# Kernel tuning notes

Measured on AMD Instinct MI355X. Metric: run time of the kernel, lower is better.

The kernel has to match this reference:

```python
import jax, jax.numpy as jnp
import numpy as np

NR, NA = 2, 1                 # num_raw, num_angle
QDIM = NR + 2 * NA            # 4: [r, x1=cos(th), x2=sin(th)]
DQ = NR + NA                  # 3: [dr, dth]
D = 2 * NR + 3 * NA           # 7: full state dim
HID = 256
EPS = 1e-6


def setup_inputs() -> dict:
    key = jax.random.key(0)
    ks = jax.random.split(key, 4)
    B = 32768
    x = jax.random.normal(ks[0], (B, D), dtype=jnp.float32)
    W0 = jax.random.normal(ks[1], (HID, D), dtype=jnp.float32) / np.sqrt(D)
    b0 = jnp.zeros((HID,), dtype=jnp.float32)
    W1 = jax.random.normal(ks[2], (HID, HID), dtype=jnp.float32) / np.sqrt(HID)
    b1 = jnp.zeros((HID,), dtype=jnp.float32)
    W2 = jax.random.normal(ks[3], (1, HID), dtype=jnp.float32) / np.sqrt(HID)
    b2 = jnp.zeros((1,), dtype=jnp.float32)
    return {"x": x, "W0": W0, "b0": b0, "W1": W1, "b1": b1, "W2": W2, "b2": b2}


def _lnn_forward(x, W0, b0, W1, b1, W2, b2):
    def L_single(xi):  # scalar Lagrangian of one state (D,)
        h = jnp.tanh(W0 @ xi + b0)
        h = jnp.tanh(W1 @ h + b1)
        return (W2 @ h + b2)[0]

    grad_single = jax.grad(L_single)
    gradL = jax.vmap(grad_single)(x)                       # (B, D)

    # Rows of the Hessian corresponding to d/d(dr,dth): (B, DQ, D).
    # Replaces the torch per-row autograd.grad loop with one batched jacfwd.
    def g(xi):
        return grad_single(xi)[QDIM:]                      # dL/d(dr,dth), (DQ,)
    Hrows = jax.vmap(jax.jacfwd(g))(x)                     # (B, DQ, D)

    x1 = x[:, NR:NR + NA]                                  # cos part (B, NA)
    x2 = x[:, NR + NA:QDIM]                                # sin part (B, NA)

    Jr = Hrows[:, :, :NR]                                  # (B, DQ, NR)
    Jx1 = Hrows[:, :, NR:NR + NA]                          # (B, DQ, NA)
    Jx2 = Hrows[:, :, NR + NA:QDIM]                        # (B, DQ, NA)
    Hdq = Hrows[:, :, QDIM:] + EPS * jnp.eye(DQ, dtype=x.dtype)  # (B, DQ, DQ)

    # chain rule back to angle theta: d/dth = -x2 * d/dx1 + x1 * d/dx2
    Jth = -x2[:, None, :] * Jx1 + x1[:, None, :] * Jx2     # (B, DQ, NA)
    Jrth = jnp.concatenate([Jr, Jth], axis=2)              # (B, DQ, DQ)

    dLdr = gradL[:, :NR]
    dLdx1 = gradL[:, NR:NR + NA]
    dLdx2 = gradL[:, NR + NA:QDIM]
    dLdth = -x2 * dLdx1 + x1 * dLdx2
    dLdrdth = jnp.concatenate([dLdr, dLdth], axis=1)       # (B, DQ)

    dq = x[:, QDIM:]                                       # (B, DQ)
    dq_term = jnp.einsum('bij,bj->bi', Jrth, dq)

    rhs = dLdrdth - dq_term                                # control = 0 (no controlNet)
    ddq = jnp.linalg.solve(Hdq, rhs[..., None])[..., 0]    # (B, DQ)

    dr = dq[:, :NR]
    dth = dq[:, NR:]
    dx1 = -x2 * dth
    dx2 = x1 * dth
    return jnp.concatenate([dr, dx1, dx2, ddq], axis=1)    # (B, D)


def reference(x, W0, b0, W1, b1, W2, b2):
    return _lnn_forward(x, W0, b0, W1, b1, W2, b2)
```

## Files before the change

### kernel.cpp

```cpp
#include <hip/hip_runtime.h>
#include <math.h>

#define HID 256
#define EPS_REG 1e-6

typedef __attribute__((ext_vector_type(8))) short short8;
typedef __attribute__((ext_vector_type(4))) short short4v;
typedef __attribute__((ext_vector_type(4))) float v4f;

#define MFMA_BF16(a, b, c) __builtin_amdgcn_mfma_f32_16x16x32_bf16((a), (b), (c), 0, 0, 0)

__device__ __forceinline__ float rtn_bf16(float v, short* s) {
    unsigned u = __float_as_uint(v);
    unsigned r = (u + 0x7FFFu + ((u >> 16) & 1u)) & 0xFFFF0000u;
    *s = (short)(r >> 16);
    return __uint_as_float(r);
}
__device__ __forceinline__ void split3(float v, short* a, short* b, short* c) {
    float f0 = rtn_bf16(v, a);
    float r1 = v - f0;
    float f1 = rtn_bf16(r1, b);
    float r2 = r1 - f1;
    (void)rtn_bf16(r2, c);
}

__global__ void prep_w1_frags(const float* __restrict__ W1, short* __restrict__ ws) {
    const int gid   = blockIdx.x * 64 + threadIdx.x;
    const int lane  = gid & 63;
    const int ks    = (gid >> 6) & 7;
    const int rt    = (gid >> 9) & 15;
    const int which = gid >> 13;
    const int m = lane & 15, q = lane >> 4;

    float v[8];
    if (which == 0) {
        const float* p = W1 + (size_t)(rt*16 + m)*HID + ks*32 + q*8;
#pragma unroll
        for (int t = 0; t < 8; ++t) v[t] = p[t];
    } else {
        const float* p = W1 + (size_t)(ks*32 + q*8)*HID + rt*16 + m;
#pragma unroll
        for (int t = 0; t < 8; ++t) v[t] = p[(size_t)t*HID];
    }
    short8 h8, m8, l8;
#pragma unroll
    for (int t = 0; t < 8; ++t) {
        short sh, sm, sl;
        split3(v[t], &sh, &sm, &sl);
        h8[t] = sh; m8[t] = sm; l8[t] = sl;
    }
    const size_t base = (size_t)which*3*65536 + ((size_t)(rt*8 + ks)*64 + lane)*8;
    *(short8*)(ws + base)          = h8;
    *(short8*)(ws + base + 65536)  = m8;
    *(short8*)(ws + base + 131072) = l8;
}

#define FRAG_NT_STRIDE 13056
#define FRAG_BUF_STRIDE 4352

__global__ __launch_bounds__(512, 4)
void lnn_mfma(const float* __restrict__ x,
              const float* __restrict__ W0, const float* __restrict__ b0,
              const float* __restrict__ b1, const float* __restrict__ W2,
              const short* __restrict__ ws,
              float* __restrict__ out)
{
    __shared__ __align__(16) short Bfrag[26112];
    __shared__ float M0h[HID * 9];

    const int tid   = threadIdx.x;
    const int samp0 = blockIdx.x * 8;
    const int lane  = tid & 63;
    const int w     = tid >> 6;

    {
        const int j  = tid & 255;
        const int s0 = (tid >> 8) * 4;
        float w0r[7];
#pragma unroll
        for (int d = 0; d < 7; ++d) w0r[d] = W0[j*7 + d];
        const float bj = b0[j];
        const int kbase = (j >> 3)*136 + (j & 7);
#pragma unroll
        for (int si = 0; si < 4; ++si) {
            const int s = s0 + si;
            const float* xs = x + (size_t)(samp0 + s)*7;
            float z = bj;
#pragma unroll
            for (int d = 0; d < 7; ++d) z = fmaf(w0r[d], xs[d], z);
            const float h  = tanhf(z);
            const float sg = 1.0f - h*h;
            M0h[j*9 + s] = h;
            const int nt = s >> 2;
            const int cb = (s & 3) * 4;
            float vals[4] = {h, sg*w0r[4], sg*w0r[5], sg*w0r[6]};
#pragma unroll
            for (int comp = 0; comp < 4; ++comp) {
                short sh, sm, sl;
                split3(vals[comp], &sh, &sm, &sl);
                const int a = nt*FRAG_NT_STRIDE + kbase + (cb + comp)*8;
                Bfrag[a]                    = sh;
                Bfrag[a + FRAG_BUF_STRIDE]  = sm;
                Bfrag[a + 2*FRAG_BUF_STRIDE]= sl;
            }
        }
    }
    __syncthreads();

    const short8* A1h = (const short8*)ws;
    const short8* A1m = A1h + 8192;
    const short8* A1l = A1h + 16384;
    const short8* A2h = A1h + 24576;
    const short8* A2m = A1h + 32768;
    const short8* A2l = A1h + 40960;

    const int q = lane >> 4;
    const int c = lane & 15;
    const int boff = q*136 + c*8;

    v4f acc[2][2];
#pragma unroll
    for (int rtl = 0; rtl < 2; ++rtl)
#pragma unroll
        for (int nt = 0; nt < 2; ++nt) acc[rtl][nt] = (v4f){0.f, 0.f, 0.f, 0.f};

#pragma unroll
    for (int ks = 0; ks < 8; ++ks) {
        short8 bh[2], bm[2], bl[2];
#pragma unroll
        for (int nt = 0; nt < 2; ++nt) {
            const int a = nt*FRAG_NT_STRIDE + ks*544 + boff;
            bh[nt] = *(const short8*)(&Bfrag[a]);
            bm[nt] = *(const short8*)(&Bfrag[a + FRAG_BUF_STRIDE]);
            bl[nt] = *(const short8*)(&Bfrag[a + 2*FRAG_BUF_STRIDE]);
        }
#pragma unroll
        for (int rtl = 0; rtl < 2; ++rtl) {
            const size_t fi = ((size_t)((w*2 + rtl)*8 + ks))*64 + lane;
            const short8 ah = A1h[fi];
            const short8 am = A1m[fi];
            const short8 al = A1l[fi];
#pragma unroll
            for (int nt = 0; nt < 2; ++nt) {
                acc[rtl][nt] = MFMA_BF16(ah, bl[nt], acc[rtl][nt]);
                acc[rtl][nt] = MFMA_BF16(al, bh[nt], acc[rtl][nt]);
                acc[rtl][nt] = MFMA_BF16(am, bm[nt], acc[rtl][nt]);
                acc[rtl][nt] = MFMA_BF16(am, bh[nt], acc[rtl][nt]);
                acc[rtl][nt] = MFMA_BF16(ah, bm[nt], acc[rtl][nt]);
                acc[rtl][nt] = MFMA_BF16(ah, bh[nt], acc[rtl][nt]);
            }
        }
    }
    __syncthreads();

    {
        const int myreg = c & 3;
#pragma unroll
        for (int rtl = 0; rtl < 2; ++rtl) {
            const int base = (w*2 + rtl)*16;
            float b1r[4], w2r[4];
#pragma unroll
            for (int r = 0; r < 4; ++r) {
                b1r[r] = b1[base + q*4 + r];
                w2r[r] = W2[base + q*4 + r];
            }
            const int G  = (base >> 3) + (q >> 1);
            const int tq = (q & 1) * 4;
#pragma unroll
            for (int nt = 0; nt < 2; ++nt) {
                float z0r[4];
#pragma unroll
                for (int r = 0; r < 4; ++r)
                    z0r[r] = __shfl(acc[rtl][nt][r] + b1r[r], lane & ~3, 64);
                const float h1m = tanhf(z0r[myreg]);
                float h1r[4];
#pragma unroll
                for (int r = 0; r < 4; ++r)
                    h1r[r] = __shfl(h1m, (lane & ~3) + r, 64);
                short4v ph, pm, pl;
#pragma unroll
                for (int r = 0; r < 4; ++r) {
                    const float h1 = h1r[r];
                    const float s1 = 1.0f - h1*h1;
                    const float av = acc[rtl][nt][r];
                    const float u  = (myreg == 0) ? (w2r[r]*s1)
                                                  : (-2.0f*w2r[r]*h1*s1)*av;
                    short sh, sm, sl;
                    split3(u, &sh, &sm, &sl);
                    ph[r] = sh; pm[r] = sm; pl[r] = sl;
                }
                const int a = nt*FRAG_NT_STRIDE + G*136 + c*8 + tq;
                *(short4v*)(&Bfrag[a])                     = ph;
                *(short4v*)(&Bfrag[a + FRAG_BUF_STRIDE])   = pm;
                *(short4v*)(&Bfrag[a + 2*FRAG_BUF_STRIDE]) = pl;
            }
        }
    }
    __syncthreads();

    v4f acc2[2][2];
#pragma unroll
    for (int rtl = 0; rtl < 2; ++rtl)
#pragma unroll
        for (int nt = 0; nt < 2; ++nt) acc2[rtl][nt] = (v4f){0.f, 0.f, 0.f, 0.f};

#pragma unroll
    for (int ks = 0; ks < 8; ++ks) {
        short8 bh[2], bm[2], bl[2];
#pragma unroll
        for (int nt = 0; nt < 2; ++nt) {
            const int a = nt*FRAG_NT_STRIDE + ks*544 + boff;
            bh[nt] = *(const short8*)(&Bfrag[a]);
            bm[nt] = *(const short8*)(&Bfrag[a + FRAG_BUF_STRIDE]);
            bl[nt] = *(const short8*)(&Bfrag[a + 2*FRAG_BUF_STRIDE]);
        }
#pragma unroll
        for (int rtl = 0; rtl < 2; ++rtl) {
            const size_t fi = ((size_t)((w*2 + rtl)*8 + ks))*64 + lane;
            const short8 ah = A2h[fi];
            const short8 am = A2m[fi];
            const short8 al = A2l[fi];
#pragma unroll
            for (int nt = 0; nt < 2; ++nt) {
                acc2[rtl][nt] = MFMA_BF16(ah, bl[nt], acc2[rtl][nt]);
                acc2[rtl][nt] = MFMA_BF16(al, bh[nt], acc2[rtl][nt]);
                acc2[rtl][nt] = MFMA_BF16(am, bm[nt], acc2[rtl][nt]);
                acc2[rtl][nt] = MFMA_BF16(am, bh[nt], acc2[rtl][nt]);
                acc2[rtl][nt] = MFMA_BF16(ah, bm[nt], acc2[rtl][nt]);
                acc2[rtl][nt] = MFMA_BF16(ah, bh[nt], acc2[rtl][nt]);
            }
        }
    }
    __syncthreads();

    {
        float* U0 = (float*)Bfrag;
#pragma unroll
        for (int rtl = 0; rtl < 2; ++rtl) {
#pragma unroll
            for (int reg = 0; reg < 4; ++reg) {
                const int j = (w*2 + rtl)*16 + q*4 + reg;
                const float w0sel = W0[j*7 + 3 + (c & 3)];
#pragma unroll
                for (int nt = 0; nt < 2; ++nt) {
                    const int s = nt*4 + (c >> 2);
                    const float pv = acc2[rtl][nt][reg];
                    const float p0 = __shfl(pv, lane & ~3, 64);
                    const float h0 = M0h[j*9 + s];
                    const float sg = 1.0f - h0*h0;
                    const float t2 = -2.0f * p0 * h0 * sg;
                    const float res = ((c & 3) == 0) ? (p0*sg)
                                                     : fmaf(pv, sg, t2 * w0sel);
                    U0[j*36 + s*4 + (c & 3)] = res;
                }
            }
        }
    }
    __syncthreads();

    const float* U0 = (const float*)Bfrag;
    const int s = tid >> 6;
    const int t = tid & 63;
    float part[25];
#pragma unroll
    for (int qq = 0; qq < 25; ++qq) part[qq] = 0.0f;

#pragma unroll
    for (int m = 0; m < 4; ++m) {
        const int j = t + 64*m;
        const float4 uv = *(const float4*)(&U0[j*36 + s*4]);
        float w0d[7];
#pragma unroll
        for (int d = 0; d < 7; ++d) w0d[d] = W0[j*7 + d];
#pragma unroll
        for (int d = 0; d < 4; ++d) part[d] = fmaf(uv.x, w0d[d], part[d]);
#pragma unroll
        for (int d = 0; d < 7; ++d) {
            part[4  + d] = fmaf(uv.y, w0d[d], part[4  + d]);
            part[11 + d] = fmaf(uv.z, w0d[d], part[11 + d]);
            part[18 + d] = fmaf(uv.w, w0d[d], part[18 + d]);
        }
    }
#pragma unroll
    for (int off = 32; off >= 1; off >>= 1)
#pragma unroll
        for (int qq = 0; qq < 25; ++qq)
            part[qq] += __shfl_xor(part[qq], off, 64);

    if (t == 0) {
        const float* xs = x + (size_t)(samp0 + s)*7;
        const double x1 = xs[2], x2 = xs[3];
        const double dq0 = xs[4], dq1 = xs[5], dth = xs[6];

        double A[3][4];
#pragma unroll
        for (int i = 0; i < 3; ++i) {
            const double J0 = part[4 + i*7 + 0];
            const double J1 = part[4 + i*7 + 1];
            const double J2 = -x2*(double)part[4 + i*7 + 2] + x1*(double)part[4 + i*7 + 3];
            const double dL = (i == 0) ? (double)part[0]
                            : (i == 1) ? (double)part[1]
                            : (-x2*(double)part[2] + x1*(double)part[3]);
            A[i][0] = (double)part[4 + i*7 + 4] + (i == 0 ? EPS_REG : 0.0);
            A[i][1] = (double)part[4 + i*7 + 5] + (i == 1 ? EPS_REG : 0.0);
            A[i][2] = (double)part[4 + i*7 + 6] + (i == 2 ? EPS_REG : 0.0);
            A[i][3] = dL - (J0*dq0 + J1*dq1 + J2*dth);
        }
        for (int cc = 0; cc < 2; ++cc) {
            int piv = cc;
            double mx = fabs(A[cc][cc]);
            for (int rr = cc + 1; rr < 3; ++rr) {
                const double v = fabs(A[rr][cc]);
                if (v > mx) { mx = v; piv = rr; }
            }
            if (piv != cc) {
                for (int k2 = 0; k2 < 4; ++k2) {
                    const double tmp = A[cc][k2]; A[cc][k2] = A[piv][k2]; A[piv][k2] = tmp;
                }
            }
            const double inv = 1.0 / A[cc][cc];
            for (int rr = cc + 1; rr < 3; ++rr) {
                const double f = A[rr][cc] * inv;
                for (int k2 = cc + 1; k2 < 4; ++k2) A[rr][k2] -= f * A[cc][k2];
            }
        }
        const double sol2 = A[2][3] / A[2][2];
        const double sol1 = (A[1][3] - A[1][2]*sol2) / A[1][1];
        const double sol0 = (A[0][3] - A[0][1]*sol1 - A[0][2]*sol2) / A[0][0];

        float* o = out + (size_t)(samp0 + s)*7;
        o[0] = (float)dq0;
        o[1] = (float)dq1;
        o[2] = (float)(-x2*dth);
        o[3] = (float)( x1*dth);
        o[4] = (float)sol0;
        o[5] = (float)sol1;
        o[6] = (float)sol2;
    }
}

#define TS8 8
#define SCP 36

__global__ void transpose_w1(const float* __restrict__ W1, float* __restrict__ W1T) {
    __shared__ float tile[32][33];
    const int bx = blockIdx.x & 7;
    const int by = blockIdx.x >> 3;
    const int tx = threadIdx.x & 31;
    const int ty = threadIdx.x >> 5;
#pragma unroll
    for (int q = 0; q < 4; ++q)
        tile[ty + q*8][tx] = W1[(by*32 + ty + q*8)*HID + bx*32 + tx];
    __syncthreads();
#pragma unroll
    for (int q = 0; q < 4; ++q)
        W1T[(bx*32 + ty + q*8)*HID + by*32 + tx] = tile[tx][ty + q*8];
}

__global__ __launch_bounds__(256, 2)
void lnn_fused(const float* __restrict__ x,
               const float* __restrict__ W0, const float* __restrict__ b0,
               const float* __restrict__ W1, const float* __restrict__ b1,
               const float* __restrict__ W2,
               const float* __restrict__ W1T, const int useT,
               float* __restrict__ out)
{
    __shared__ float M0[HID * SCP];
    __shared__ float U [HID * SCP];
    const int tid   = threadIdx.x;
    const int samp0 = blockIdx.x * TS8;
    {
        const int j = tid;
        float w0r[7];
#pragma unroll
        for (int d = 0; d < 7; ++d) w0r[d] = W0[j*7 + d];
        const float bj = b0[j];
#pragma unroll
        for (int s = 0; s < TS8; ++s) {
            const float* xs = x + (size_t)(samp0 + s)*7;
            float z = bj;
#pragma unroll
            for (int d = 0; d < 7; ++d) z = fmaf(w0r[d], xs[d], z);
            const float h  = tanhf(z);
            const float sg = 1.0f - h*h;
            float4 v = {h, sg * w0r[4], sg * w0r[5], sg * w0r[6]};
            *(float4*)(&M0[j*SCP + s*4]) = v;
        }
    }
    __syncthreads();
    const int it = tid & 63;
    const int ct = tid >> 6;
    float acc[4][8];
#pragma unroll
    for (int r = 0; r < 4; ++r)
#pragma unroll
        for (int c = 0; c < 8; ++c) acc[r][c] = 0.0f;
    if (useT) {
#pragma unroll 4
        for (int j = 0; j < HID; ++j) {
            const float4 w4 = *(const float4*)(W1T + (size_t)j*HID + it*4);
            const float4 ma = *(const float4*)(&M0[j*SCP + ct*8]);
            const float4 mb = *(const float4*)(&M0[j*SCP + ct*8 + 4]);
            const float w[4] = {w4.x, w4.y, w4.z, w4.w};
            const float m[8] = {ma.x, ma.y, ma.z, ma.w, mb.x, mb.y, mb.z, mb.w};
#pragma unroll
            for (int r = 0; r < 4; ++r)
#pragma unroll
                for (int c = 0; c < 8; ++c)
                    acc[r][c] = fmaf(w[r], m[c], acc[r][c]);
        }
    } else {
#pragma unroll 2
        for (int j = 0; j < HID; ++j) {
            float w[4];
#pragma unroll
            for (int r = 0; r < 4; ++r) w[r] = W1[(size_t)(it*4 + r)*HID + j];
            const float4 ma = *(const float4*)(&M0[j*SCP + ct*8]);
            const float4 mb = *(const float4*)(&M0[j*SCP + ct*8 + 4]);
            const float m[8] = {ma.x, ma.y, ma.z, ma.w, mb.x, mb.y, mb.z, mb.w};
#pragma unroll
            for (int r = 0; r < 4; ++r)
#pragma unroll
                for (int c = 0; c < 8; ++c)
                    acc[r][c] = fmaf(w[r], m[c], acc[r][c]);
        }
    }
    {
#pragma unroll
        for (int r = 0; r < 4; ++r) {
            const int i = it*4 + r;
            const float b1i = b1[i];
            const float w2i = W2[i];
#pragma unroll
            for (int cs = 0; cs < 2; ++cs) {
                const float z1 = acc[r][cs*4+0] + b1i;
                const float h1 = tanhf(z1);
                const float s1 = 1.0f - h1*h1;
                float4 uv;
                uv.x = w2i * s1;
                const float m2 = -2.0f * w2i * h1 * s1;
                uv.y = m2 * acc[r][cs*4+1];
                uv.z = m2 * acc[r][cs*4+2];
                uv.w = m2 * acc[r][cs*4+3];
                *(float4*)(&U[i*SCP + ct*8 + cs*4]) = uv;
            }
        }
    }
    __syncthreads();
    float acc2[4][8];
#pragma unroll
    for (int r = 0; r < 4; ++r)
#pragma unroll
        for (int c = 0; c < 8; ++c) acc2[r][c] = 0.0f;
#pragma unroll 4
    for (int i = 0; i < HID; ++i) {
        const float4 w4 = *(const float4*)(W1 + (size_t)i*HID + it*4);
        const float4 ua = *(const float4*)(&U[i*SCP + ct*8]);
        const float4 ub = *(const float4*)(&U[i*SCP + ct*8 + 4]);
        const float w[4] = {w4.x, w4.y, w4.z, w4.w};
        const float m[8] = {ua.x, ua.y, ua.z, ua.w, ub.x, ub.y, ub.z, ub.w};
#pragma unroll
        for (int r = 0; r < 4; ++r)
#pragma unroll
            for (int c = 0; c < 8; ++c)
                acc2[r][c] = fmaf(w[r], m[c], acc2[r][c]);
    }
    __syncthreads();
    {
#pragma unroll
        for (int r = 0; r < 4; ++r) {
            const int j = it*4 + r;
#pragma unroll
            for (int cs = 0; cs < 2; ++cs) {
                const int scb = ct*8 + cs*4;
                const float4 mm = *(const float4*)(&M0[j*SCP + scb]);
                const float h0v = mm.x;
                const float sg  = 1.0f - h0v*h0v;
                const float p   = acc2[r][cs*4+0];
                const float t2  = -2.0f * p * h0v;
                float4 uv;
                uv.x = p * sg;
                uv.y = fmaf(acc2[r][cs*4+1], sg, t2 * mm.y);
                uv.z = fmaf(acc2[r][cs*4+2], sg, t2 * mm.z);
                uv.w = fmaf(acc2[r][cs*4+3], sg, t2 * mm.w);
                *(float4*)(&U[j*SCP + scb]) = uv;
            }
        }
    }
    __syncthreads();
    const int s = tid >> 5;
    const int t = tid & 31;
    float part[25];
#pragma unroll
    for (int qq = 0; qq < 25; ++qq) part[qq] = 0.0f;
#pragma unroll
    for (int m = 0; m < 8; ++m) {
        const int j = t + 32*m;
        const float4 uv = *(const float4*)(&U[j*SCP + s*4]);
        float w0d[7];
#pragma unroll
        for (int d = 0; d < 7; ++d) w0d[d] = W0[j*7 + d];
#pragma unroll
        for (int d = 0; d < 4; ++d) part[d] = fmaf(uv.x, w0d[d], part[d]);
#pragma unroll
        for (int d = 0; d < 7; ++d) {
            part[4  + d] = fmaf(uv.y, w0d[d], part[4  + d]);
            part[11 + d] = fmaf(uv.z, w0d[d], part[11 + d]);
            part[18 + d] = fmaf(uv.w, w0d[d], part[18 + d]);
        }
    }
#pragma unroll
    for (int off = 16; off >= 1; off >>= 1)
#pragma unroll
        for (int qq = 0; qq < 25; ++qq)
            part[qq] += __shfl_xor(part[qq], off, 64);
    if (t == 0) {
        const float* xs = x + (size_t)(samp0 + s)*7;
        const double x1 = xs[2], x2 = xs[3];
        const double dq0 = xs[4], dq1 = xs[5], dth = xs[6];
        double A[3][4];
#pragma unroll
        for (int i = 0; i < 3; ++i) {
            const double J0 = part[4 + i*7 + 0];
            const double J1 = part[4 + i*7 + 1];
            const double J2 = -x2*(double)part[4 + i*7 + 2] + x1*(double)part[4 + i*7 + 3];
            const double dL = (i == 0) ? (double)part[0]
                            : (i == 1) ? (double)part[1]
                            : (-x2*(double)part[2] + x1*(double)part[3]);
            A[i][0] = (double)part[4 + i*7 + 4] + (i == 0 ? EPS_REG : 0.0);
            A[i][1] = (double)part[4 + i*7 + 5] + (i == 1 ? EPS_REG : 0.0);
            A[i][2] = (double)part[4 + i*7 + 6] + (i == 2 ? EPS_REG : 0.0);
            A[i][3] = dL - (J0*dq0 + J1*dq1 + J2*dth);
        }
        for (int cc = 0; cc < 2; ++cc) {
            int piv = cc;
            double mx = fabs(A[cc][cc]);
            for (int rr = cc + 1; rr < 3; ++rr) {
                const double v = fabs(A[rr][cc]);
                if (v > mx) { mx = v; piv = rr; }
            }
            if (piv != cc) {
                for (int k2 = 0; k2 < 4; ++k2) {
                    const double tmp = A[cc][k2]; A[cc][k2] = A[piv][k2]; A[piv][k2] = tmp;
                }
            }
            const double inv = 1.0 / A[cc][cc];
            for (int rr = cc + 1; rr < 3; ++rr) {
                const double f = A[rr][cc] * inv;
                for (int k2 = cc + 1; k2 < 4; ++k2) A[rr][k2] -= f * A[cc][k2];
            }
        }
        const double sol2 = A[2][3] / A[2][2];
        const double sol1 = (A[1][3] - A[1][2]*sol2) / A[1][1];
        const double sol0 = (A[0][3] - A[0][1]*sol1 - A[0][2]*sol2) / A[0][0];
        float* o = out + (size_t)(samp0 + s)*7;
        o[0] = (float)dq0;
        o[1] = (float)dq1;
        o[2] = (float)(-x2*dth);
        o[3] = (float)( x1*dth);
        o[4] = (float)sol0;
        o[5] = (float)sol1;
        o[6] = (float)sol2;
    }
}

extern "C" void kernel_launch(void* const* d_in, const int* in_sizes, int n_in,
                              void* d_out, int out_size, void* d_ws, size_t ws_size,
                              hipStream_t stream) {
    const float* x  = (const float*)d_in[0];
    const float* W0 = (const float*)d_in[1];
    const float* b0 = (const float*)d_in[2];
    const float* W1 = (const float*)d_in[3];
    const float* b1 = (const float*)d_in[4];
    const float* W2 = (const float*)d_in[5];
    float* out = (float*)d_out;

    const int B = in_sizes[0] / 7;
    const size_t NEED = 6u * 65536u * sizeof(short);

    if (ws_size >= NEED && (B % 8) == 0) {
        short* ws = (short*)d_ws;
        prep_w1_frags<<<256, 64, 0, stream>>>(W1, ws);
        lnn_mfma<<<B / 8, 512, 0, stream>>>(x, W0, b0, b1, W2, ws, out);
    } else {
        const int useT = (ws_size >= (size_t)HID * HID * sizeof(float)) ? 1 : 0;
        float* W1T = (float*)d_ws;
        if (useT) transpose_w1<<<64, 256, 0, stream>>>(W1, W1T);
        lnn_fused<<<B / TS8, 256, 0, stream>>>(x, W0, b0, W1, b1, W2, W1T, useT, out);
    }
}
```

Measured before the change: 300.1 us.

## Prefetch A fragments, reduce via LDS scratch, use cofactor solve, simplify rounding

The W1/W2 fragment loads from global memory are double-buffered across k-steps so the next step's A fragments load while the current MFMAs run. The 64-lane shuffle reduction of 25 partials is cut to two shuffle steps, with the rest summed through an LDS scratch area. The pivoted Gaussian elimination becomes a closed-form 3x3 cofactor/determinant solve, and bf16 rounding switches from round-to-nearest-even to a cheaper round-half-up. The prefetch raises register pressure, the cofactor solve drops pivoting, and the scratch writes lack an explicit barrier, which relies on intra-wave ordering.

```diff
diff --git a/kernel.cpp b/kernel.cpp
--- a/kernel.cpp
+++ b/kernel.cpp
@@ -11,8 +11,7 @@
 #define MFMA_BF16(a, b, c) __builtin_amdgcn_mfma_f32_16x16x32_bf16((a), (b), (c), 0, 0, 0)
 
 __device__ __forceinline__ float rtn_bf16(float v, short* s) {
-    unsigned u = __float_as_uint(v);
-    unsigned r = (u + 0x7FFFu + ((u >> 16) & 1u)) & 0xFFFF0000u;
+    unsigned r = (__float_as_uint(v) + 0x8000u) & 0xFFFF0000u;
     *s = (short)(r >> 16);
     return __uint_as_float(r);
 }
@@ -124,30 +123,45 @@
 #pragma unroll
         for (int nt = 0; nt < 2; ++nt) acc[rtl][nt] = (v4f){0.f, 0.f, 0.f, 0.f};
 
-#pragma unroll
-    for (int ks = 0; ks < 8; ++ks) {
-        short8 bh[2], bm[2], bl[2];
-#pragma unroll
-        for (int nt = 0; nt < 2; ++nt) {
-            const int a = nt*FRAG_NT_STRIDE + ks*544 + boff;
-            bh[nt] = *(const short8*)(&Bfrag[a]);
-            bm[nt] = *(const short8*)(&Bfrag[a + FRAG_BUF_STRIDE]);
-            bl[nt] = *(const short8*)(&Bfrag[a + 2*FRAG_BUF_STRIDE]);
-        }
+    {
+        short8 pah[2][2], pam[2][2], pal[2][2];
 #pragma unroll
         for (int rtl = 0; rtl < 2; ++rtl) {
-            const size_t fi = ((size_t)((w*2 + rtl)*8 + ks))*64 + lane;
-            const short8 ah = A1h[fi];
-            const short8 am = A1m[fi];
-            const short8 al = A1l[fi];
+            const size_t fi = ((size_t)((w*2 + rtl)*8))*64 + lane;
+            pah[0][rtl] = A1h[fi]; pam[0][rtl] = A1m[fi]; pal[0][rtl] = A1l[fi];
+        }
+#pragma unroll
+        for (int ks = 0; ks < 8; ++ks) {
+            const int cur = ks & 1, nxt = cur ^ 1;
+            if (ks < 7) {
+#pragma unroll
+                for (int rtl = 0; rtl < 2; ++rtl) {
+                    const size_t fi = ((size_t)((w*2 + rtl)*8 + ks + 1))*64 + lane;
+                    pah[nxt][rtl] = A1h[fi]; pam[nxt][rtl] = A1m[fi]; pal[nxt][rtl] = A1l[fi];
+                }
+            }
+            short8 bh[2], bm[2], bl[2];
 #pragma unroll
             for (int nt = 0; nt < 2; ++nt) {
-                acc[rtl][nt] = MFMA_BF16(ah, bl[nt], acc[rtl][nt]);
-                acc[rtl][nt] = MFMA_BF16(al, bh[nt], acc[rtl][nt]);
-                acc[rtl][nt] = MFMA_BF16(am, bm[nt], acc[rtl][nt]);
-                acc[rtl][nt] = MFMA_BF16(am, bh[nt], acc[rtl][nt]);
-                acc[rtl][nt] = MFMA_BF16(ah, bm[nt], acc[rtl][nt]);
-                acc[rtl][nt] = MFMA_BF16(ah, bh[nt], acc[rtl][nt]);
+                const int a = nt*FRAG_NT_STRIDE + ks*544 + boff;
+                bh[nt] = *(const short8*)(&Bfrag[a]);
+                bm[nt] = *(const short8*)(&Bfrag[a + FRAG_BUF_STRIDE]);
+                bl[nt] = *(const short8*)(&Bfrag[a + 2*FRAG_BUF_STRIDE]);
+            }
+#pragma unroll
+            for (int rtl = 0; rtl < 2; ++rtl) {
+                const short8 ah = pah[cur][rtl];
+                const short8 am = pam[cur][rtl];
+                const short8 al = pal[cur][rtl];
+#pragma unroll
+                for (int nt = 0; nt < 2; ++nt) {
+                    acc[rtl][nt] = MFMA_BF16(ah, bl[nt], acc[rtl][nt]);
+                    acc[rtl][nt] = MFMA_BF16(al, bh[nt], acc[rtl][nt]);
+                    acc[rtl][nt] = MFMA_BF16(am, bm[nt], acc[rtl][nt]);
+                    acc[rtl][nt] = MFMA_BF16(am, bh[nt], acc[rtl][nt]);
+                    acc[rtl][nt] = MFMA_BF16(ah, bm[nt], acc[rtl][nt]);
+                    acc[rtl][nt] = MFMA_BF16(ah, bh[nt], acc[rtl][nt]);
+                }
             }
         }
     }
@@ -204,30 +218,45 @@
 #pragma unroll
         for (int nt = 0; nt < 2; ++nt) acc2[rtl][nt] = (v4f){0.f, 0.f, 0.f, 0.f};
 
-#pragma unroll
-    for (int ks = 0; ks < 8; ++ks) {
-        short8 bh[2], bm[2], bl[2];
-#pragma unroll
-        for (int nt = 0; nt < 2; ++nt) {
-            const int a = nt*FRAG_NT_STRIDE + ks*544 + boff;
-            bh[nt] = *(const short8*)(&Bfrag[a]);
-            bm[nt] = *(const short8*)(&Bfrag[a + FRAG_BUF_STRIDE]);
-            bl[nt] = *(const short8*)(&Bfrag[a + 2*FRAG_BUF_STRIDE]);
-        }
+    {
+        short8 pah[2][2], pam[2][2], pal[2][2];
 #pragma unroll
         for (int rtl = 0; rtl < 2; ++rtl) {
-            const size_t fi = ((size_t)((w*2 + rtl)*8 + ks))*64 + lane;
-            const short8 ah = A2h[fi];
-            const short8 am = A2m[fi];
-            const short8 al = A2l[fi];
+            const size_t fi = ((size_t)((w*2 + rtl)*8))*64 + lane;
+            pah[0][rtl] = A2h[fi]; pam[0][rtl] = A2m[fi]; pal[0][rtl] = A2l[fi];
+        }
+#pragma unroll
+        for (int ks = 0; ks < 8; ++ks) {
+            const int cur = ks & 1, nxt = cur ^ 1;
+            if (ks < 7) {
+#pragma unroll
+                for (int rtl = 0; rtl < 2; ++rtl) {
+                    const size_t fi = ((size_t)((w*2 + rtl)*8 + ks + 1))*64 + lane;
+                    pah[nxt][rtl] = A2h[fi]; pam[nxt][rtl] = A2m[fi]; pal[nxt][rtl] = A2l[fi];
+                }
+            }
+            short8 bh[2], bm[2], bl[2];
 #pragma unroll
             for (int nt = 0; nt < 2; ++nt) {
-                acc2[rtl][nt] = MFMA_BF16(ah, bl[nt], acc2[rtl][nt]);
-                acc2[rtl][nt] = MFMA_BF16(al, bh[nt], acc2[rtl][nt]);
-                acc2[rtl][nt] = MFMA_BF16(am, bm[nt], acc2[rtl][nt]);
-                acc2[rtl][nt] = MFMA_BF16(am, bh[nt], acc2[rtl][nt]);
-                acc2[rtl][nt] = MFMA_BF16(ah, bm[nt], acc2[rtl][nt]);
-                acc2[rtl][nt] = MFMA_BF16(ah, bh[nt], acc2[rtl][nt]);
+                const int a = nt*FRAG_NT_STRIDE + ks*544 + boff;
+                bh[nt] = *(const short8*)(&Bfrag[a]);
+                bm[nt] = *(const short8*)(&Bfrag[a + FRAG_BUF_STRIDE]);
+                bl[nt] = *(const short8*)(&Bfrag[a + 2*FRAG_BUF_STRIDE]);
+            }
+#pragma unroll
+            for (int rtl = 0; rtl < 2; ++rtl) {
+                const short8 ah = pah[cur][rtl];
+                const short8 am = pam[cur][rtl];
+                const short8 al = pal[cur][rtl];
+#pragma unroll
+                for (int nt = 0; nt < 2; ++nt) {
+                    acc2[rtl][nt] = MFMA_BF16(ah, bl[nt], acc2[rtl][nt]);
+                    acc2[rtl][nt] = MFMA_BF16(al, bh[nt], acc2[rtl][nt]);
+                    acc2[rtl][nt] = MFMA_BF16(am, bm[nt], acc2[rtl][nt]);
+                    acc2[rtl][nt] = MFMA_BF16(am, bh[nt], acc2[rtl][nt]);
+                    acc2[rtl][nt] = MFMA_BF16(ah, bm[nt], acc2[rtl][nt]);
+                    acc2[rtl][nt] = MFMA_BF16(ah, bh[nt], acc2[rtl][nt]);
+                }
             }
         }
     }
@@ -259,7 +288,8 @@
     __syncthreads();
 
     const float* U0 = (const float*)Bfrag;
-    const int s = tid >> 6;
+    float* scratch = ((float*)Bfrag) + 9216 + w * 425;
+    const int s = w;
     const int t = tid & 63;
     float part[25];
 #pragma unroll
@@ -282,51 +312,62 @@
         }
     }
 #pragma unroll
-    for (int off = 32; off >= 1; off >>= 1)
+    for (int off = 1; off <= 2; off <<= 1)
 #pragma unroll
         for (int qq = 0; qq < 25; ++qq)
             part[qq] += __shfl_xor(part[qq], off, 64);
+    {
+        const int quad = t >> 2;
+        if ((t & 3) == 0) {
+#pragma unroll
+            for (int e = 0; e < 25; ++e)
+                scratch[e*17 + quad] = part[e];
+        }
+    }
+    if (t < 25) {
+        float tot = 0.0f;
+#pragma unroll
+        for (int k = 0; k < 16; ++k) tot += scratch[t*17 + k];
+        scratch[t*17 + 16] = tot;
+    }
 
     if (t == 0) {
+        double g[25];
+#pragma unroll
+        for (int e = 0; e < 25; ++e) g[e] = (double)scratch[e*17 + 16];
+
         const float* xs = x + (size_t)(samp0 + s)*7;
         const double x1 = xs[2], x2 = xs[3];
         const double dq0 = xs[4], dq1 = xs[5], dth = xs[6];
 
-        double A[3][4];
+        double M[3][3], rhs[3];
 #pragma unroll
         for (int i = 0; i < 3; ++i) {
-            const double J0 = part[4 + i*7 + 0];
-            const double J1 = part[4 + i*7 + 1];
-            const double J2 = -x2*(double)part[4 + i*7 + 2] + x1*(double)part[4 + i*7 + 3];
-            const double dL = (i == 0) ? (double)part[0]
-                            : (i == 1) ? (double)part[1]
-                            : (-x2*(double)part[2] + x1*(double)part[3]);
-            A[i][0] = (double)part[4 + i*7 + 4] + (i == 0 ? EPS_REG : 0.0);
-            A[i][1] = (double)part[4 + i*7 + 5] + (i == 1 ? EPS_REG : 0.0);
-            A[i][2] = (double)part[4 + i*7 + 6] + (i == 2 ? EPS_REG : 0.0);
-            A[i][3] = dL - (J0*dq0 + J1*dq1 + J2*dth);
-        }
-        for (int cc = 0; cc < 2; ++cc) {
-            int piv = cc;
-            double mx = fabs(A[cc][cc]);
-            for (int rr = cc + 1; rr < 3; ++rr) {
-                const double v = fabs(A[rr][cc]);
-                if (v > mx) { mx = v; piv = rr; }
-            }
-            if (piv != cc) {
-                for (int k2 = 0; k2 < 4; ++k2) {
-                    const double tmp = A[cc][k2]; A[cc][k2] = A[piv][k2]; A[piv][k2] = tmp;
-                }
-            }
-            const double inv = 1.0 / A[cc][cc];
-            for (int rr = cc + 1; rr < 3; ++rr) {
-                const double f = A[rr][cc] * inv;
-                for (int k2 = cc + 1; k2 < 4; ++k2) A[rr][k2] -= f * A[cc][k2];
-            }
-        }
-        const double sol2 = A[2][3] / A[2][2];
-        const double sol1 = (A[1][3] - A[1][2]*sol2) / A[1][1];
-        const double sol0 = (A[0][3] - A[0][1]*sol1 - A[0][2]*sol2) / A[0][0];
+            const double J0 = g[4 + i*7 + 0];
+            const double J1 = g[4 + i*7 + 1];
+            const double J2 = -x2*g[4 + i*7 + 2] + x1*g[4 + i*7 + 3];
+            const double dL = (i == 0) ? g[0]
+                            : (i == 1) ? g[1]
+                            : (-x2*g[2] + x1*g[3]);
+            M[i][0] = g[4 + i*7 + 4] + (i == 0 ? EPS_REG : 0.0);
+            M[i][1] = g[4 + i*7 + 5] + (i == 1 ? EPS_REG : 0.0);
+            M[i][2] = g[4 + i*7 + 6] + (i == 2 ? EPS_REG : 0.0);
+            rhs[i]  = dL - (J0*dq0 + J1*dq1 + J2*dth);
+        }
+        const double c00 = M[1][1]*M[2][2] - M[1][2]*M[2][1];
+        const double c01 = M[1][2]*M[2][0] - M[1][0]*M[2][2];
+        const double c02 = M[1][0]*M[2][1] - M[1][1]*M[2][0];
+        const double det = M[0][0]*c00 + M[0][1]*c01 + M[0][2]*c02;
+        const double inv = 1.0 / det;
+        const double c10 = M[0][2]*M[2][1] - M[0][1]*M[2][2];
+        const double c11 = M[0][0]*M[2][2] - M[0][2]*M[2][0];
+        const double c12 = M[0][1]*M[2][0] - M[0][0]*M[2][1];
+        const double c20 = M[0][1]*M[1][2] - M[0][2]*M[1][1];
+        const double c21 = M[0][2]*M[1][0] - M[0][0]*M[1][2];
+        const double c22 = M[0][0]*M[1][1] - M[0][1]*M[1][0];
+        const double sol0 = (c00*rhs[0] + c10*rhs[1] + c20*rhs[2]) * inv;
+        const double sol1 = (c01*rhs[0] + c11*rhs[1] + c21*rhs[2]) * inv;
+        const double sol2 = (c02*rhs[0] + c12*rhs[1] + c22*rhs[2]) * inv;
 
         float* o = out + (size_t)(samp0 + s)*7;
         o[0] = (float)dq0;
```

Measured after the change: 274.2 us. -8.6%, faster.
